# Kernel optimization log

Measured on AMD Instinct MI355X. Metric: run time of the kernel, lower is better.

The kernel has to match this reference:

```python
import jax, jax.numpy as jnp
import numpy as np

A1, A2 = 16, 16            # block tile sizes (arr_size1, arr_size2)
G = 1000                   # graph_size (max node index + 1)
EG = 16000                 # number of graph edges (avg degree 16)
SIZE1 = G * A1             # input feature length  (16000)
SIZE2 = G * A2             # output feature length (16000)
NNZ = EG * A1 * A2         # expanded COO entries  (4,096,000)
B = 32                     # batch


def _expand_indices(t0, t1, a1, a2):
    """Vectorized adjust_indices: edge (t0,t1) -> tile of (row,col) pairs.
    row = t0*a2 + j, col = t1*a1 + i  for all i in [a1), j in [a2)."""
    e = t0.shape[0]
    j = np.arange(a2)
    i = np.arange(a1)
    rows = np.broadcast_to(t0[:, None, None] * a2 + j[None, None, :], (e, a1, a2)).reshape(-1)
    cols = np.broadcast_to(t1[:, None, None] * a1 + i[None, :, None], (e, a1, a2)).reshape(-1)
    return rows.astype(np.int32), cols.astype(np.int32)


def setup_inputs() -> dict:
    key = jax.random.key(0)
    ks = jax.random.split(key, 6)
    rng = np.random.default_rng(0)
    t0 = rng.integers(0, G, EG)
    t1 = rng.integers(0, G, EG)
    rows_np, cols_np = _expand_indices(t0, t1, A1, A2)
    # original init: uniform(-1/len(indices), 1/len(indices)) with len([2,nnz])==2 -> U(-0.5, 0.5)
    return {
        "x": jax.random.normal(ks[0], (B, SIZE1, 1), dtype=jnp.float32),
        "weight_mean": jax.random.uniform(ks[1], (NNZ,), jnp.float32, -0.5, 0.5),
        "weight_log_var": jnp.zeros((NNZ,), jnp.float32),
        "b_mean": jax.random.uniform(ks[2], (SIZE2,), jnp.float32, -0.5, 0.5),
        "b_log_var": jnp.zeros((SIZE2,), jnp.float32),
        "eps_w": jax.random.normal(ks[3], (NNZ,), dtype=jnp.float32),
        "eps_b": jax.random.normal(ks[4], (SIZE2,), dtype=jnp.float32),
        "rows": jnp.asarray(rows_np),
        "cols": jnp.asarray(cols_np),
    }


def reference(x, weight_mean, weight_log_var, b_mean, b_log_var, eps_w, eps_b, rows, cols):
    # reparameterization sample of sparse weight values
    values = eps_w * jnp.exp(weight_log_var) + weight_mean          # [NNZ]
    # COO spmm: out[b, r, k] += values[e] * x[b, c, k] for each (r, c) = (rows[e], cols[e])
    contrib = values[None, :, None] * x[:, cols, :]                 # [B, NNZ, 1]
    out = jnp.zeros((x.shape[0], SIZE2, x.shape[2]), x.dtype).at[:, rows, :].add(contrib)
    # reparameterized bias, broadcast over batch
    b = eps_b * jnp.exp(b_log_var) + b_mean                         # [SIZE2]
    out = out + b[None, :, None]
    # kl is explicitly zeroed in the source right before return
    return (out, jnp.asarray(0.0, dtype=x.dtype))
```

## Files before the change

### kernel.cpp

```cpp
#include <hip/hip_runtime.h>

#define EG   16000
#define NG   1000
#define BB   32
#define SIZE 16000
#define CAP  64

typedef float f32x4 __attribute__((ext_vector_type(4)));

__global__ __launch_bounds__(256) void pack_kernel(
    const int* __restrict__ rows, const int* __restrict__ cols,
    int* __restrict__ pk)
{
    int e = blockIdx.x * 256 + threadIdx.x;
    if (e < EG) {
        int t0 = rows[(long)e << 8] >> 4;
        int t1 = cols[(long)e << 8] >> 4;
        pk[e] = (t0 << 10) | t1;
    }
}

__global__ __launch_bounds__(256, 4) void spmm_kernel(
    const float* __restrict__ wm, const float* __restrict__ wlv,
    const float* __restrict__ ew, const float* __restrict__ x,
    const float* __restrict__ bm, const float* __restrict__ blv,
    const float* __restrict__ eb, const int* __restrict__ pk,
    float* __restrict__ out)
{
    __shared__ f32x4 vt[2][4][64];
    __shared__ f32x4 xs[2][4][160];
    __shared__ int   sl[CAP];
    __shared__ int   scnt;

    int g   = blockIdx.x;
    int tid = threadIdx.x;

    if (tid == 0) scnt = 0;
    __syncthreads();
    const int4* pk4 = (const int4*)pk;
    for (int c = tid; c < EG / 4; c += 256) {
        int4 v = pk4[c];
        int e0 = c << 2;
        if ((v.x >> 10) == g) { int p = atomicAdd(&scnt, 1); if (p < CAP) sl[p] = ((e0    ) << 10) | (v.x & 1023); }
        if ((v.y >> 10) == g) { int p = atomicAdd(&scnt, 1); if (p < CAP) sl[p] = ((e0 + 1) << 10) | (v.y & 1023); }
        if ((v.z >> 10) == g) { int p = atomicAdd(&scnt, 1); if (p < CAP) sl[p] = ((e0 + 2) << 10) | (v.z & 1023); }
        if ((v.w >> 10) == g) { int p = atomicAdd(&scnt, 1); if (p < CAP) sl[p] = ((e0 + 3) << 10) | (v.w & 1023); }
    }
    __syncthreads();
    int n = scnt; n = n < CAP ? n : CAP;

    int wave = tid >> 6;
    int lane = tid & 63;
    int jg   = lane & 3;
    int cb2  = lane >> 2;

    f32x4 acc0 = {0.f,0.f,0.f,0.f}, acc1 = {0.f,0.f,0.f,0.f};
    f32x4 m4, l4, g4, xv0, xv1;
    int iters = (n + 3) >> 2;
    bool vcur = false, vnxt = false;

    auto issue = [&](int idx) -> bool {
        bool val = idx < n;
        if (val) {
            int pkv = sl[idx];
            int e   = pkv >> 10;
            int t1  = pkv & 1023;
            long wq = ((long)e << 6) + lane;
            m4 = ((const f32x4*)wm)[wq];
            l4 = ((const f32x4*)wlv)[wq];
            g4 = ((const f32x4*)ew)[wq];
            const f32x4* x4 = (const f32x4*)x;
            int c0 = lane, c1 = lane + 64;
            xv0 = x4[(long)(c0 >> 2) * (SIZE/4) + (t1 << 2) + (c0 & 3)];
            xv1 = x4[(long)(c1 >> 2) * (SIZE/4) + (t1 << 2) + (c1 & 3)];
        }
        return val;
    };
    auto writeb = [&](int buf, bool val) {
        if (val) {
            f32x4 v;
            v.x = g4.x * __expf(l4.x) + m4.x;
            v.y = g4.y * __expf(l4.y) + m4.y;
            v.z = g4.z * __expf(l4.z) + m4.z;
            v.w = g4.w * __expf(l4.w) + m4.w;
            vt[buf][wave][lane] = v;
            int c0 = lane, c1 = lane + 64;
            xs[buf][wave][(c0 >> 2) * 5 + (c0 & 3)] = xv0;
            xs[buf][wave][(c1 >> 2) * 5 + (c1 & 3)] = xv1;
        }
    };
    auto compute = [&](int buf, bool val) {
        if (!val) return;
        f32x4 a0 = xs[buf][wave][ cb2       * 5 + 0];
        f32x4 a1 = xs[buf][wave][ cb2       * 5 + 1];
        f32x4 a2 = xs[buf][wave][ cb2       * 5 + 2];
        f32x4 a3 = xs[buf][wave][ cb2       * 5 + 3];
        f32x4 b0 = xs[buf][wave][(cb2 + 16) * 5 + 0];
        f32x4 b1 = xs[buf][wave][(cb2 + 16) * 5 + 1];
        f32x4 b2 = xs[buf][wave][(cb2 + 16) * 5 + 2];
        f32x4 b3 = xs[buf][wave][(cb2 + 16) * 5 + 3];
        float xra[16] = {a0.x,a0.y,a0.z,a0.w, a1.x,a1.y,a1.z,a1.w,
                         a2.x,a2.y,a2.z,a2.w, a3.x,a3.y,a3.z,a3.w};
        float xrb[16] = {b0.x,b0.y,b0.z,b0.w, b1.x,b1.y,b1.z,b1.w,
                         b2.x,b2.y,b2.z,b2.w, b3.x,b3.y,b3.z,b3.w};
        #pragma unroll
        for (int i = 0; i < 16; ++i) {
            f32x4 w = vt[buf][wave][(i << 2) + jg];
            acc0 += w * xra[i];
            acc1 += w * xrb[i];
        }
    };

    vcur = issue(wave);
    writeb(0, vcur);
    __syncthreads();
    for (int it = 0; it < iters; ++it) {
        bool more = (it + 1 < iters);
        if (more) vnxt = issue(((it + 1) << 2) + wave);
        compute(it & 1, vcur);
        if (more) writeb((it + 1) & 1, vnxt);
        __syncthreads();
        vcur = vnxt;
    }

    f32x4* sred = &xs[0][0][0];
    sred[(wave << 7) + (lane << 1) + 0] = acc0;
    sred[(wave << 7) + (lane << 1) + 1] = acc1;
    __syncthreads();
    if (tid < 128) {
        int cb  = tid >> 2;
        int jgf = tid & 3;
        int h   = cb >> 4;
        int sl_ = ((cb & 15) << 2) + jgf;
        f32x4 s = sred[(0 << 7) + (sl_ << 1) + h]
                + sred[(1 << 7) + (sl_ << 1) + h]
                + sred[(2 << 7) + (sl_ << 1) + h]
                + sred[(3 << 7) + (sl_ << 1) + h];
        int r0 = (g << 4) + (jgf << 2);
        f32x4 b4 = *(const f32x4*)&bm[r0];
        f32x4 v4 = *(const f32x4*)&blv[r0];
        f32x4 e4 = *(const f32x4*)&eb[r0];
        f32x4 o;
        o.x = s.x + (e4.x * __expf(v4.x) + b4.x);
        o.y = s.y + (e4.y * __expf(v4.y) + b4.y);
        o.z = s.z + (e4.z * __expf(v4.z) + b4.z);
        o.w = s.w + (e4.w * __expf(v4.w) + b4.w);
        *(f32x4*)&out[(long)cb * SIZE + r0] = o;
    }
    if (g == 0 && tid == 0) out[(long)BB * SIZE] = 0.0f;
}

extern "C" void kernel_launch(void* const* d_in, const int* in_sizes, int n_in,
                              void* d_out, int out_size, void* d_ws, size_t ws_size,
                              hipStream_t stream) {
    const float* x   = (const float*)d_in[0];
    const float* wm  = (const float*)d_in[1];
    const float* wlv = (const float*)d_in[2];
    const float* bm  = (const float*)d_in[3];
    const float* blv = (const float*)d_in[4];
    const float* ew  = (const float*)d_in[5];
    const float* eb  = (const float*)d_in[6];
    const int* rows  = (const int*)d_in[7];
    const int* cols  = (const int*)d_in[8];
    float* out = (float*)d_out;

    int* pk = (int*)d_ws;

    pack_kernel<<<(EG + 255) / 256, 256, 0, stream>>>(rows, cols, pk);
    spmm_kernel<<<NG, 256, 0, stream>>>(wm, wlv, ew, x, bm, blv, eb, pk, out);
}
```

Baseline: 133.0 us.

## Split batch across two blocks per output node to double grid parallelism

Each output node row is now handled by two blocks, each covering 16 of the 32 batch columns, which doubles the grid to 2000 blocks and halves per-thread accumulators and shared memory. Launch bounds are raised to allow more resident blocks. The cost is that every block rescans the packed edge list and recomputes the weight reparameterization (exp) and weight loads, doubling that work and its memory traffic.

```diff
diff --git a/kernel.cpp b/kernel.cpp
--- a/kernel.cpp
+++ b/kernel.cpp
@@ -20,7 +20,7 @@
     }
 }
 
-__global__ __launch_bounds__(256, 4) void spmm_kernel(
+__global__ __launch_bounds__(256, 8) void spmm_kernel(
     const float* __restrict__ wm, const float* __restrict__ wlv,
     const float* __restrict__ ew, const float* __restrict__ x,
     const float* __restrict__ bm, const float* __restrict__ blv,
@@ -28,12 +28,15 @@
     float* __restrict__ out)
 {
     __shared__ f32x4 vt[2][4][64];
-    __shared__ f32x4 xs[2][4][160];
+    __shared__ f32x4 xs[2][4][80];
     __shared__ int   sl[CAP];
     __shared__ int   scnt;
 
-    int g   = blockIdx.x;
-    int tid = threadIdx.x;
+    int bid  = blockIdx.x;
+    int half = bid / 1000;
+    int g    = bid - half * 1000;
+    int tid  = threadIdx.x;
+    int bb0  = half << 4;
 
     if (tid == 0) scnt = 0;
     __syncthreads();
@@ -52,10 +55,10 @@
     int wave = tid >> 6;
     int lane = tid & 63;
     int jg   = lane & 3;
-    int cb2  = lane >> 2;
+    int cb   = lane >> 2;
 
-    f32x4 acc0 = {0.f,0.f,0.f,0.f}, acc1 = {0.f,0.f,0.f,0.f};
-    f32x4 m4, l4, g4, xv0, xv1;
+    f32x4 acc = {0.f, 0.f, 0.f, 0.f};
+    f32x4 m4, l4, g4, xv0;
     int iters = (n + 3) >> 2;
     bool vcur = false, vnxt = false;
 
@@ -70,9 +73,8 @@
             l4 = ((const f32x4*)wlv)[wq];
             g4 = ((const f32x4*)ew)[wq];
             const f32x4* x4 = (const f32x4*)x;
-            int c0 = lane, c1 = lane + 64;
-            xv0 = x4[(long)(c0 >> 2) * (SIZE/4) + (t1 << 2) + (c0 & 3)];
-            xv1 = x4[(long)(c1 >> 2) * (SIZE/4) + (t1 << 2) + (c1 & 3)];
+            int lb = lane >> 2, q = lane & 3;
+            xv0 = x4[(long)(bb0 + lb) * (SIZE/4) + (t1 << 2) + q];
         }
         return val;
     };
@@ -84,30 +86,22 @@
             v.z = g4.z * __expf(l4.z) + m4.z;
             v.w = g4.w * __expf(l4.w) + m4.w;
             vt[buf][wave][lane] = v;
-            int c0 = lane, c1 = lane + 64;
-            xs[buf][wave][(c0 >> 2) * 5 + (c0 & 3)] = xv0;
-            xs[buf][wave][(c1 >> 2) * 5 + (c1 & 3)] = xv1;
+            int lb = lane >> 2, q = lane & 3;
+            xs[buf][wave][lb * 5 + q] = xv0;
         }
     };
     auto compute = [&](int buf, bool val) {
         if (!val) return;
-        f32x4 a0 = xs[buf][wave][ cb2       * 5 + 0];
-        f32x4 a1 = xs[buf][wave][ cb2       * 5 + 1];
-        f32x4 a2 = xs[buf][wave][ cb2       * 5 + 2];
-        f32x4 a3 = xs[buf][wave][ cb2       * 5 + 3];
-        f32x4 b0 = xs[buf][wave][(cb2 + 16) * 5 + 0];
-        f32x4 b1 = xs[buf][wave][(cb2 + 16) * 5 + 1];
-        f32x4 b2 = xs[buf][wave][(cb2 + 16) * 5 + 2];
-        f32x4 b3 = xs[buf][wave][(cb2 + 16) * 5 + 3];
-        float xra[16] = {a0.x,a0.y,a0.z,a0.w, a1.x,a1.y,a1.z,a1.w,
-                         a2.x,a2.y,a2.z,a2.w, a3.x,a3.y,a3.z,a3.w};
-        float xrb[16] = {b0.x,b0.y,b0.z,b0.w, b1.x,b1.y,b1.z,b1.w,
-                         b2.x,b2.y,b2.z,b2.w, b3.x,b3.y,b3.z,b3.w};
+        f32x4 x0 = xs[buf][wave][cb * 5 + 0];
+        f32x4 x1 = xs[buf][wave][cb * 5 + 1];
+        f32x4 x2 = xs[buf][wave][cb * 5 + 2];
+        f32x4 x3 = xs[buf][wave][cb * 5 + 3];
+        float xr[16] = {x0.x,x0.y,x0.z,x0.w, x1.x,x1.y,x1.z,x1.w,
+                        x2.x,x2.y,x2.z,x2.w, x3.x,x3.y,x3.z,x3.w};
         #pragma unroll
         for (int i = 0; i < 16; ++i) {
             f32x4 w = vt[buf][wave][(i << 2) + jg];
-            acc0 += w * xra[i];
-            acc1 += w * xrb[i];
+            acc += w * xr[i];
         }
     };
 
@@ -124,18 +118,13 @@
     }
 
     f32x4* sred = &xs[0][0][0];
-    sred[(wave << 7) + (lane << 1) + 0] = acc0;
-    sred[(wave << 7) + (lane << 1) + 1] = acc1;
+    sred[(wave << 6) + lane] = acc;
     __syncthreads();
-    if (tid < 128) {
-        int cb  = tid >> 2;
+    if (tid < 64) {
+        int cbf = tid >> 2;
         int jgf = tid & 3;
-        int h   = cb >> 4;
-        int sl_ = ((cb & 15) << 2) + jgf;
-        f32x4 s = sred[(0 << 7) + (sl_ << 1) + h]
-                + sred[(1 << 7) + (sl_ << 1) + h]
-                + sred[(2 << 7) + (sl_ << 1) + h]
-                + sred[(3 << 7) + (sl_ << 1) + h];
+        f32x4 s = sred[(0 << 6) + tid] + sred[(1 << 6) + tid]
+                + sred[(2 << 6) + tid] + sred[(3 << 6) + tid];
         int r0 = (g << 4) + (jgf << 2);
         f32x4 b4 = *(const f32x4*)&bm[r0];
         f32x4 v4 = *(const f32x4*)&blv[r0];
@@ -145,9 +134,9 @@
         o.y = s.y + (e4.y * __expf(v4.y) + b4.y);
         o.z = s.z + (e4.z * __expf(v4.z) + b4.z);
         o.w = s.w + (e4.w * __expf(v4.w) + b4.w);
-        *(f32x4*)&out[(long)cb * SIZE + r0] = o;
+        *(f32x4*)&out[(long)(bb0 + cbf) * SIZE + r0] = o;
     }
-    if (g == 0 && tid == 0) out[(long)BB * SIZE] = 0.0f;
+    if (bid == 0 && tid == 0) out[(long)BB * SIZE] = 0.0f;
 }
 
 extern "C" void kernel_launch(void* const* d_in, const int* in_sizes, int n_in,
@@ -167,5 +156,5 @@
     int* pk = (int*)d_ws;
 
     pack_kernel<<<(EG + 255) / 256, 256, 0, stream>>>(rows, cols, pk);
-    spmm_kernel<<<NG, 256, 0, stream>>>(wm, wlv, ew, x, bm, blv, eb, pk, out);
+    spmm_kernel<<<2 * NG, 256, 0, stream>>>(wm, wlv, ew, x, bm, blv, eb, pk, out);
 }
```

Result: no change. 134.4 us (+1.0%).

## Partition edge scan per wave and drop block-wide barriers in main loop

Applied to the files above, without the earlier changes.

Each wave now scans its own quarter of the packed edge list, builds a private edge list with its own counter, and processes those edges with per-wave double buffers. No __syncthreads is needed during the scan or the pipelined loop, only before the final cross-wave reduction. This removes block barriers and shared-atomic contention across waves. The cost is possible load imbalance between waves and a lower per-wave cap of 32 edges, which could drop edges if one wave's slice holds more than that. The loop also relies on same-wave LDS ordering without explicit wave barriers.

```diff
diff --git a/kernel.cpp b/kernel.cpp
--- a/kernel.cpp
+++ b/kernel.cpp
@@ -4,7 +4,7 @@
 #define NG   1000
 #define BB   32
 #define SIZE 16000
-#define CAP  64
+#define CAPW 32
 
 typedef float f32x4 __attribute__((ext_vector_type(4)));
 
@@ -27,102 +27,90 @@
     const float* __restrict__ eb, const int* __restrict__ pk,
     float* __restrict__ out)
 {
-    __shared__ f32x4 vt[2][4][64];
-    __shared__ f32x4 xs[2][4][160];
-    __shared__ int   sl[CAP];
-    __shared__ int   scnt;
+    __shared__ f32x4 vt[4][2][64];
+    __shared__ f32x4 xs[4][2][160];
+    __shared__ int   sl[4][CAPW];
+    __shared__ int   scnt[4];
 
-    int g   = blockIdx.x;
-    int tid = threadIdx.x;
+    int g    = blockIdx.x;
+    int tid  = threadIdx.x;
+    int wave = tid >> 6;
+    int lane = tid & 63;
 
-    if (tid == 0) scnt = 0;
-    __syncthreads();
+    if (lane == 0) scnt[wave] = 0;
+
     const int4* pk4 = (const int4*)pk;
-    for (int c = tid; c < EG / 4; c += 256) {
+    int base = wave * 1000;
+    for (int c = base + lane; c < base + 1000; c += 64) {
         int4 v = pk4[c];
         int e0 = c << 2;
-        if ((v.x >> 10) == g) { int p = atomicAdd(&scnt, 1); if (p < CAP) sl[p] = ((e0    ) << 10) | (v.x & 1023); }
-        if ((v.y >> 10) == g) { int p = atomicAdd(&scnt, 1); if (p < CAP) sl[p] = ((e0 + 1) << 10) | (v.y & 1023); }
-        if ((v.z >> 10) == g) { int p = atomicAdd(&scnt, 1); if (p < CAP) sl[p] = ((e0 + 2) << 10) | (v.z & 1023); }
-        if ((v.w >> 10) == g) { int p = atomicAdd(&scnt, 1); if (p < CAP) sl[p] = ((e0 + 3) << 10) | (v.w & 1023); }
+        if ((v.x >> 10) == g) { int p = atomicAdd(&scnt[wave], 1); if (p < CAPW) sl[wave][p] = ((e0    ) << 10) | (v.x & 1023); }
+        if ((v.y >> 10) == g) { int p = atomicAdd(&scnt[wave], 1); if (p < CAPW) sl[wave][p] = ((e0 + 1) << 10) | (v.y & 1023); }
+        if ((v.z >> 10) == g) { int p = atomicAdd(&scnt[wave], 1); if (p < CAPW) sl[wave][p] = ((e0 + 2) << 10) | (v.z & 1023); }
+        if ((v.w >> 10) == g) { int p = atomicAdd(&scnt[wave], 1); if (p < CAPW) sl[wave][p] = ((e0 + 3) << 10) | (v.w & 1023); }
     }
-    __syncthreads();
-    int n = scnt; n = n < CAP ? n : CAP;
+    int nw = scnt[wave];
+    nw = nw < CAPW ? nw : CAPW;
 
-    int wave = tid >> 6;
-    int lane = tid & 63;
-    int jg   = lane & 3;
-    int cb2  = lane >> 2;
+    int jg  = lane & 3;
+    int cb2 = lane >> 2;
 
     f32x4 acc0 = {0.f,0.f,0.f,0.f}, acc1 = {0.f,0.f,0.f,0.f};
     f32x4 m4, l4, g4, xv0, xv1;
-    int iters = (n + 3) >> 2;
-    bool vcur = false, vnxt = false;
 
-    auto issue = [&](int idx) -> bool {
-        bool val = idx < n;
-        if (val) {
-            int pkv = sl[idx];
-            int e   = pkv >> 10;
-            int t1  = pkv & 1023;
-            long wq = ((long)e << 6) + lane;
-            m4 = ((const f32x4*)wm)[wq];
-            l4 = ((const f32x4*)wlv)[wq];
-            g4 = ((const f32x4*)ew)[wq];
-            const f32x4* x4 = (const f32x4*)x;
-            int c0 = lane, c1 = lane + 64;
-            xv0 = x4[(long)(c0 >> 2) * (SIZE/4) + (t1 << 2) + (c0 & 3)];
-            xv1 = x4[(long)(c1 >> 2) * (SIZE/4) + (t1 << 2) + (c1 & 3)];
-        }
-        return val;
+    auto issue = [&](int idx) {
+        int pkv = sl[wave][idx];
+        int e   = pkv >> 10;
+        int t1  = pkv & 1023;
+        long wq = ((long)e << 6) + lane;
+        m4 = ((const f32x4*)wm)[wq];
+        l4 = ((const f32x4*)wlv)[wq];
+        g4 = ((const f32x4*)ew)[wq];
+        const f32x4* x4 = (const f32x4*)x;
+        int c0 = lane, c1 = lane + 64;
+        xv0 = x4[(long)(c0 >> 2) * (SIZE/4) + (t1 << 2) + (c0 & 3)];
+        xv1 = x4[(long)(c1 >> 2) * (SIZE/4) + (t1 << 2) + (c1 & 3)];
     };
-    auto writeb = [&](int buf, bool val) {
-        if (val) {
-            f32x4 v;
-            v.x = g4.x * __expf(l4.x) + m4.x;
-            v.y = g4.y * __expf(l4.y) + m4.y;
-            v.z = g4.z * __expf(l4.z) + m4.z;
-            v.w = g4.w * __expf(l4.w) + m4.w;
-            vt[buf][wave][lane] = v;
-            int c0 = lane, c1 = lane + 64;
-            xs[buf][wave][(c0 >> 2) * 5 + (c0 & 3)] = xv0;
-            xs[buf][wave][(c1 >> 2) * 5 + (c1 & 3)] = xv1;
-        }
+    auto writeb = [&](int buf) {
+        f32x4 v;
+        v.x = g4.x * __expf(l4.x) + m4.x;
+        v.y = g4.y * __expf(l4.y) + m4.y;
+        v.z = g4.z * __expf(l4.z) + m4.z;
+        v.w = g4.w * __expf(l4.w) + m4.w;
+        vt[wave][buf][lane] = v;
+        int c0 = lane, c1 = lane + 64;
+        xs[wave][buf][(c0 >> 2) * 5 + (c0 & 3)] = xv0;
+        xs[wave][buf][(c1 >> 2) * 5 + (c1 & 3)] = xv1;
     };
-    auto compute = [&](int buf, bool val) {
-        if (!val) return;
-        f32x4 a0 = xs[buf][wave][ cb2       * 5 + 0];
-        f32x4 a1 = xs[buf][wave][ cb2       * 5 + 1];
-        f32x4 a2 = xs[buf][wave][ cb2       * 5 + 2];
-        f32x4 a3 = xs[buf][wave][ cb2       * 5 + 3];
-        f32x4 b0 = xs[buf][wave][(cb2 + 16) * 5 + 0];
-        f32x4 b1 = xs[buf][wave][(cb2 + 16) * 5 + 1];
-        f32x4 b2 = xs[buf][wave][(cb2 + 16) * 5 + 2];
-        f32x4 b3 = xs[buf][wave][(cb2 + 16) * 5 + 3];
+    auto compute = [&](int buf) {
+        f32x4 a0 = xs[wave][buf][ cb2       * 5 + 0];
+        f32x4 a1 = xs[wave][buf][ cb2       * 5 + 1];
+        f32x4 a2 = xs[wave][buf][ cb2       * 5 + 2];
+        f32x4 a3 = xs[wave][buf][ cb2       * 5 + 3];
+        f32x4 b0 = xs[wave][buf][(cb2 + 16) * 5 + 0];
+        f32x4 b1 = xs[wave][buf][(cb2 + 16) * 5 + 1];
+        f32x4 b2 = xs[wave][buf][(cb2 + 16) * 5 + 2];
+        f32x4 b3 = xs[wave][buf][(cb2 + 16) * 5 + 3];
         float xra[16] = {a0.x,a0.y,a0.z,a0.w, a1.x,a1.y,a1.z,a1.w,
                          a2.x,a2.y,a2.z,a2.w, a3.x,a3.y,a3.z,a3.w};
         float xrb[16] = {b0.x,b0.y,b0.z,b0.w, b1.x,b1.y,b1.z,b1.w,
                          b2.x,b2.y,b2.z,b2.w, b3.x,b3.y,b3.z,b3.w};
         #pragma unroll
         for (int i = 0; i < 16; ++i) {
-            f32x4 w = vt[buf][wave][(i << 2) + jg];
+            f32x4 w = vt[wave][buf][(i << 2) + jg];
             acc0 += w * xra[i];
             acc1 += w * xrb[i];
         }
     };
 
-    vcur = issue(wave);
-    writeb(0, vcur);
-    __syncthreads();
-    for (int it = 0; it < iters; ++it) {
-        bool more = (it + 1 < iters);
-        if (more) vnxt = issue(((it + 1) << 2) + wave);
-        compute(it & 1, vcur);
-        if (more) writeb((it + 1) & 1, vnxt);
-        __syncthreads();
-        vcur = vnxt;
+    if (nw > 0) { issue(0); writeb(0); }
+    for (int it = 0; it < nw; ++it) {
+        if (it + 1 < nw) issue(it + 1);
+        compute(it & 1);
+        if (it + 1 < nw) writeb((it + 1) & 1);
     }
 
+    __syncthreads();
     f32x4* sred = &xs[0][0][0];
     sred[(wave << 7) + (lane << 1) + 0] = acc0;
     sred[(wave << 7) + (lane << 1) + 1] = acc1;
```

Result: slower. 161.6 us (+21.5%).

## Precompute sampled weights in a streaming pre-pass; simplify SpMM inner loop

Applied to the files above, without the earlier changes.

The weight reparameterization (eps*exp(logvar)+mean) moves out of the SpMM kernel into a coalesced pre-pass. The pre-pass uses nontemporal loads and writes the sampled values to workspace, along with the packed edge indices. The SpMM kernel then loads one array per edge instead of three, which shortens its per-iteration gather latency and register pressure. The inner compute loop is also restructured to read x in float4 chunks directly from LDS instead of staging 32 scalars in registers. The cost is an extra 16MB write and read of the value array through global memory.

```diff
diff --git a/kernel.cpp b/kernel.cpp
--- a/kernel.cpp
+++ b/kernel.cpp
@@ -8,21 +8,30 @@
 
 typedef float f32x4 __attribute__((ext_vector_type(4)));
 
-__global__ __launch_bounds__(256) void pack_kernel(
-    const int* __restrict__ rows, const int* __restrict__ cols,
-    int* __restrict__ pk)
+__global__ __launch_bounds__(256) void gather_kernel(
+    const float* __restrict__ wm, const float* __restrict__ wlv,
+    const float* __restrict__ ew, const int* __restrict__ rows,
+    const int* __restrict__ cols, float* __restrict__ v, int* __restrict__ pk)
 {
-    int e = blockIdx.x * 256 + threadIdx.x;
-    if (e < EG) {
-        int t0 = rows[(long)e << 8] >> 4;
-        int t1 = cols[(long)e << 8] >> 4;
-        pk[e] = (t0 << 10) | t1;
-    }
+    int t = blockIdx.x * 256 + threadIdx.x;
+    const f32x4* wm4  = (const f32x4*)wm;
+    const f32x4* wlv4 = (const f32x4*)wlv;
+    const f32x4* ew4  = (const f32x4*)ew;
+    f32x4 m4 = __builtin_nontemporal_load(&wm4[t]);
+    f32x4 l4 = __builtin_nontemporal_load(&wlv4[t]);
+    f32x4 g4 = __builtin_nontemporal_load(&ew4[t]);
+    f32x4 o;
+    o.x = g4.x * __expf(l4.x) + m4.x;
+    o.y = g4.y * __expf(l4.y) + m4.y;
+    o.z = g4.z * __expf(l4.z) + m4.z;
+    o.w = g4.w * __expf(l4.w) + m4.w;
+    ((f32x4*)v)[t] = o;
+    if (t < EG)
+        pk[t] = ((rows[(long)t << 8] >> 4) << 10) | (cols[(long)t << 8] >> 4);
 }
 
 __global__ __launch_bounds__(256, 4) void spmm_kernel(
-    const float* __restrict__ wm, const float* __restrict__ wlv,
-    const float* __restrict__ ew, const float* __restrict__ x,
+    const float* __restrict__ v, const float* __restrict__ x,
     const float* __restrict__ bm, const float* __restrict__ blv,
     const float* __restrict__ eb, const int* __restrict__ pk,
     float* __restrict__ out)
@@ -39,12 +48,12 @@
     __syncthreads();
     const int4* pk4 = (const int4*)pk;
     for (int c = tid; c < EG / 4; c += 256) {
-        int4 v = pk4[c];
+        int4 w = pk4[c];
         int e0 = c << 2;
-        if ((v.x >> 10) == g) { int p = atomicAdd(&scnt, 1); if (p < CAP) sl[p] = ((e0    ) << 10) | (v.x & 1023); }
-        if ((v.y >> 10) == g) { int p = atomicAdd(&scnt, 1); if (p < CAP) sl[p] = ((e0 + 1) << 10) | (v.y & 1023); }
-        if ((v.z >> 10) == g) { int p = atomicAdd(&scnt, 1); if (p < CAP) sl[p] = ((e0 + 2) << 10) | (v.z & 1023); }
-        if ((v.w >> 10) == g) { int p = atomicAdd(&scnt, 1); if (p < CAP) sl[p] = ((e0 + 3) << 10) | (v.w & 1023); }
+        if ((w.x >> 10) == g) { int p = atomicAdd(&scnt, 1); if (p < CAP) sl[p] = ((e0    ) << 10) | (w.x & 1023); }
+        if ((w.y >> 10) == g) { int p = atomicAdd(&scnt, 1); if (p < CAP) sl[p] = ((e0 + 1) << 10) | (w.y & 1023); }
+        if ((w.z >> 10) == g) { int p = atomicAdd(&scnt, 1); if (p < CAP) sl[p] = ((e0 + 2) << 10) | (w.z & 1023); }
+        if ((w.w >> 10) == g) { int p = atomicAdd(&scnt, 1); if (p < CAP) sl[p] = ((e0 + 3) << 10) | (w.w & 1023); }
     }
     __syncthreads();
     int n = scnt; n = n < CAP ? n : CAP;
@@ -55,7 +64,7 @@
     int cb2  = lane >> 2;
 
     f32x4 acc0 = {0.f,0.f,0.f,0.f}, acc1 = {0.f,0.f,0.f,0.f};
-    f32x4 m4, l4, g4, xv0, xv1;
+    f32x4 v4s, xv0, xv1;
     int iters = (n + 3) >> 2;
     bool vcur = false, vnxt = false;
 
@@ -65,10 +74,7 @@
             int pkv = sl[idx];
             int e   = pkv >> 10;
             int t1  = pkv & 1023;
-            long wq = ((long)e << 6) + lane;
-            m4 = ((const f32x4*)wm)[wq];
-            l4 = ((const f32x4*)wlv)[wq];
-            g4 = ((const f32x4*)ew)[wq];
+            v4s = ((const f32x4*)v)[((long)e << 6) + lane];
             const f32x4* x4 = (const f32x4*)x;
             int c0 = lane, c1 = lane + 64;
             xv0 = x4[(long)(c0 >> 2) * (SIZE/4) + (t1 << 2) + (c0 & 3)];
@@ -78,12 +84,7 @@
     };
     auto writeb = [&](int buf, bool val) {
         if (val) {
-            f32x4 v;
-            v.x = g4.x * __expf(l4.x) + m4.x;
-            v.y = g4.y * __expf(l4.y) + m4.y;
-            v.z = g4.z * __expf(l4.z) + m4.z;
-            v.w = g4.w * __expf(l4.w) + m4.w;
-            vt[buf][wave][lane] = v;
+            vt[buf][wave][lane] = v4s;
             int c0 = lane, c1 = lane + 64;
             xs[buf][wave][(c0 >> 2) * 5 + (c0 & 3)] = xv0;
             xs[buf][wave][(c1 >> 2) * 5 + (c1 & 3)] = xv1;
@@ -91,23 +92,18 @@
     };
     auto compute = [&](int buf, bool val) {
         if (!val) return;
-        f32x4 a0 = xs[buf][wave][ cb2       * 5 + 0];
-        f32x4 a1 = xs[buf][wave][ cb2       * 5 + 1];
-        f32x4 a2 = xs[buf][wave][ cb2       * 5 + 2];
-        f32x4 a3 = xs[buf][wave][ cb2       * 5 + 3];
-        f32x4 b0 = xs[buf][wave][(cb2 + 16) * 5 + 0];
-        f32x4 b1 = xs[buf][wave][(cb2 + 16) * 5 + 1];
-        f32x4 b2 = xs[buf][wave][(cb2 + 16) * 5 + 2];
-        f32x4 b3 = xs[buf][wave][(cb2 + 16) * 5 + 3];
-        float xra[16] = {a0.x,a0.y,a0.z,a0.w, a1.x,a1.y,a1.z,a1.w,
-                         a2.x,a2.y,a2.z,a2.w, a3.x,a3.y,a3.z,a3.w};
-        float xrb[16] = {b0.x,b0.y,b0.z,b0.w, b1.x,b1.y,b1.z,b1.w,
-                         b2.x,b2.y,b2.z,b2.w, b3.x,b3.y,b3.z,b3.w};
         #pragma unroll
-        for (int i = 0; i < 16; ++i) {
-            f32x4 w = vt[buf][wave][(i << 2) + jg];
-            acc0 += w * xra[i];
-            acc1 += w * xrb[i];
+        for (int q = 0; q < 4; ++q) {
+            f32x4 xa = xs[buf][wave][ cb2       * 5 + q];
+            f32x4 xb = xs[buf][wave][(cb2 + 16) * 5 + q];
+            f32x4 w0 = vt[buf][wave][(q << 4) + 0  + jg];
+            f32x4 w1 = vt[buf][wave][(q << 4) + 4  + jg];
+            f32x4 w2 = vt[buf][wave][(q << 4) + 8  + jg];
+            f32x4 w3 = vt[buf][wave][(q << 4) + 12 + jg];
+            acc0 += w0 * xa.x; acc0 += w1 * xa.y;
+            acc0 += w2 * xa.z; acc0 += w3 * xa.w;
+            acc1 += w0 * xb.x; acc1 += w1 * xb.y;
+            acc1 += w2 * xb.z; acc1 += w3 * xb.w;
         }
     };
 
@@ -164,8 +160,10 @@
     const int* cols  = (const int*)d_in[8];
     float* out = (float*)d_out;
 
-    int* pk = (int*)d_ws;
+    char* ws = (char*)d_ws;
+    float* v  = (float*)ws;
+    int*   pk = (int*)(ws + (size_t)EG * 256 * 4);
 
-    pack_kernel<<<(EG + 255) / 256, 256, 0, stream>>>(rows, cols, pk);
-    spmm_kernel<<<NG, 256, 0, stream>>>(wm, wlv, ew, x, bm, blv, eb, pk, out);
+    gather_kernel<<<(EG * 64) / 256, 256, 0, stream>>>(wm, wlv, ew, rows, cols, v, pk);
+    spmm_kernel<<<NG, 256, 0, stream>>>(v, x, bm, blv, eb, pk, out);
 }
```

Result: slower. 137.8 us (+3.6%).
